# Performance work log

Hardware: AMD Instinct MI355X
Metric: run time of the kernel (lower is better)

## Reference

```python
import jax, jax.numpy as jnp
import numpy as np

K = 65536          # memory bank size
P = 4096           # partition_size
D = 256            # out_dim
E = 2              # num_experts_per_concept
SMOOTH = 0.1
NUM_TASKS = 1
B = 4096


def setup_inputs() -> dict:
    key = jax.random.key(0)
    k1, k2, k3 = jax.random.split(key, 3)
    queue = jax.random.normal(k1, (D, K), dtype=jnp.float32)
    queue = queue / jnp.linalg.norm(queue, axis=0, keepdims=True)  # normalize(dim=0)
    return {
        "student_embeds": jax.random.normal(k2, (B, D), dtype=jnp.float32),
        "teacher_embeds": jax.random.normal(k3, (B, D), dtype=jnp.float32),
        "queue": queue,
        "student_temp": 0.1,
        "teacher_temp": 0.04,
    }


def _one_task(queue, student_embeds, teacher_embeds, student_temp, teacher_temp, key):
    kperm, ksel = jax.random.split(key)
    # random partition of the bank (torch.randperm + split)
    perm = jax.random.permutation(kperm, K)
    part_idx, mem_idx = perm[:P], perm[P:]
    part = queue[:, part_idx]                      # [D, P]
    mem = queue[:, mem_idx]                        # [D, K-P]
    Kmp = K - P

    sims = part.T @ mem                            # [P, K-P]
    neigh_scores, neigh_idx = jax.lax.top_k(sims, E - 1)  # [P, E-1]

    # append self index (offset into concatenated [mem | part]) and 1-smoothing score
    idx_ = jnp.concatenate([neigh_idx, (Kmp + jnp.arange(P))[:, None]], axis=1)          # [P, E]
    scores_ = jnp.concatenate(
        [neigh_scores, jnp.full((P, 1), 1.0 - SMOOTH, dtype=sims.dtype)], axis=1)        # [P, E]

    # low_energy selection: multinomial(weights, P//2, replacement=False)
    P2 = P // 2
    m = jnp.mean(neigh_scores, axis=-1)            # [P]
    sample_means = jnp.abs(m)
    sample_stds = m                                 # (faithful to source: same quantity)
    coef = (sample_stds / (sample_means + 1e-8)) * (1.0 + 1.0 / (4.0 * Kmp))
    weights = 1.0 / coef                            # [P]
    # Gumbel top-k == multinomial without replacement proportional to weights
    gumbel = jax.random.gumbel(ksel, (P,))
    sel = jax.lax.top_k(jnp.log(weights) + gumbel, P2)[1]   # [P2]
    idx_ = idx_[sel]                                # [P2, E]
    scores_ = scores_[sel]                          # [P2, E]

    embeds_ = jnp.concatenate([mem, part], axis=1)  # [D, K]
    pne = embeds_[:, idx_.reshape(-1)]              # [D, P2*E] partition_neigh_embeddings

    sf = scores_.reshape(-1)                        # [P2*E]
    smooth_val = (1.0 - sf) / (P2 - 1)              # [P2*E]
    # partition_labels = arange(P).repeat_interleave(E)[:P2*E] == repeat(arange(P2), E)
    labels = jnp.repeat(jnp.arange(P2), E)          # [P2*E]
    M = jnp.broadcast_to(smooth_val[:, None], (P2 * E, P2))
    M = M.at[jnp.arange(P2 * E), labels].set(sf)    # scatter_ on dim 1
    M = M / M.sum(-1, keepdims=True)                # row-normalize

    s_probs = jax.nn.softmax(student_embeds @ pne / student_temp, axis=-1) @ M  # [B, P2]
    t_probs = jax.nn.softmax(teacher_embeds @ pne / teacher_temp, axis=-1) @ M  # [B, P2]
    return s_probs, t_probs


def reference(student_embeds, teacher_embeds, queue, student_temp, teacher_temp):
    base = jax.random.key(42)  # internal RNG (torch.randperm / multinomial equivalents)
    s_list, t_list = [], []
    for i in range(NUM_TASKS):
        s, t = _one_task(queue, student_embeds, teacher_embeds,
                         student_temp, teacher_temp, jax.random.fold_in(base, i))
        s_list.append(s)
        t_list.append(t)
    return jnp.stack(s_list), jnp.stack(t_list)  # each [NUM_TASKS, B, P//2]
```

## Files before the change

### kernel.cpp

```cpp
#include <hip/hip_runtime.h>
#include <cstdint>
#include <cmath>
#include <cstring>
#include <vector>
#include <algorithm>
#include <utility>

#define KTOT 65536
#define PP   4096
#define DD   256
#define KMP  61440
#define P2   2048
#define BB   4096
#define NPB  512
#define INVALID_C 0xFFFFFFFFu

static inline void tf2x32(uint32_t k0, uint32_t k1, uint32_t x0, uint32_t x1,
                          uint32_t* o0, uint32_t* o1) {
  static const uint32_t rot[2][4] = {{13u,15u,26u,6u},{17u,29u,16u,24u}};
  uint32_t ks[3] = {k0, k1, 0x1BD11BDAu ^ k0 ^ k1};
  uint32_t v0 = x0 + ks[0], v1 = x1 + ks[1];
  for (int i = 0; i < 5; ++i) {
    const uint32_t* r = rot[i & 1];
    for (int j = 0; j < 4; ++j) {
      v0 += v1;
      v1 = (v1 << r[j]) | (v1 >> (32u - r[j]));
      v1 ^= v0;
    }
    v0 += ks[(i + 1) % 3];
    v1 += ks[(i + 2) % 3] + (uint32_t)(i + 1);
  }
  *o0 = v0; *o1 = v1;
}

static inline uint32_t tf_bits32(uint32_t k0, uint32_t k1, uint32_t i) {
  uint32_t a, b;
  tf2x32(k0, k1, 0u, i, &a, &b);
  return a ^ b;
}

static uint32_t h_upload[KMP + KTOT + P2];
static uint32_t* const h_mem_idx    = h_upload;
static uint32_t* const h_pos_in_mem = h_upload + KMP;
static uint32_t* const h_partsel    = h_upload + KMP + KTOT;

static void host_prepare() {
  uint32_t f0, f1; tf2x32(0u, 42u, 0u, 0u, &f0, &f1);
  uint32_t kperm0, kperm1, ksel0, ksel1;
  tf2x32(f0, f1, 0u, 0u, &kperm0, &kperm1);
  tf2x32(f0, f1, 0u, 1u, &ksel0, &ksel1);

  std::vector<uint32_t> perm(KTOT);
  for (uint32_t i = 0; i < KTOT; ++i) perm[i] = i;
  std::vector<std::pair<uint32_t,uint32_t>> kv(KTOT);
  uint32_t key0 = kperm0, key1 = kperm1;
  for (int round = 0; round < 2; ++round) {
    uint32_t nk0, nk1, sk0, sk1;
    tf2x32(key0, key1, 0u, 0u, &nk0, &nk1);
    tf2x32(key0, key1, 0u, 1u, &sk0, &sk1);
    key0 = nk0; key1 = nk1;
    for (uint32_t i = 0; i < KTOT; ++i) {
      kv[i].first  = tf_bits32(sk0, sk1, i);
      kv[i].second = perm[i];
    }
    std::stable_sort(kv.begin(), kv.end(),
        [](const std::pair<uint32_t,uint32_t>& a,
           const std::pair<uint32_t,uint32_t>& b){ return a.first < b.first; });
    for (uint32_t i = 0; i < KTOT; ++i) perm[i] = kv[i].second;
  }
  static uint32_t part_idx[PP];
  for (int i = 0; i < PP;  ++i) part_idx[i] = perm[i];
  for (int i = 0; i < KMP; ++i) h_mem_idx[i] = perm[PP + i];
  for (int i = 0; i < KTOT; ++i) h_pos_in_mem[i] = INVALID_C;
  for (uint32_t c = 0; c < KMP; ++c) h_pos_in_mem[h_mem_idx[c]] = c;

  static float sval[PP];
  float c1f = (float)(1.0 + 1.0/(4.0*(double)KMP));
  float L0  = logf(1.0f / c1f);
  for (uint32_t i = 0; i < PP; ++i) {
    uint32_t bits = tf_bits32(ksel0, ksel1, i);
    uint32_t fb = (bits >> 9) | 0x3F800000u;
    float f; memcpy(&f, &fb, 4);
    f -= 1.0f;
    float u = (f == 0.0f) ? 1.17549435e-38f : f;
    float g = -logf(-logf(u));
    sval[i] = L0 + g;
  }
  static uint32_t order[PP];
  for (uint32_t i = 0; i < PP; ++i) order[i] = i;
  std::sort(order, order + PP, [](uint32_t a, uint32_t b){
    if (sval[a] != sval[b]) return sval[a] > sval[b];
    return a < b;
  });
  for (int k = 0; k < P2; ++k) h_partsel[k] = part_idx[order[k]];

  (void)hipHostRegister((void*)h_upload, sizeof(h_upload), hipHostRegisterDefault);
}

static const bool _host_tables_ready = (host_prepare(), true);

typedef __attribute__((ext_vector_type(8))) short bf16x8;
typedef __attribute__((ext_vector_type(4))) float f32x4;

__device__ inline unsigned short f2bf(float x) {
  union { float f; uint32_t u; } v; v.f = x;
  return (unsigned short)((v.u + 0x7FFFu + ((v.u >> 16) & 1u)) >> 16);
}

__device__ inline void gload16(const unsigned short* g, unsigned short* l) {
  __builtin_amdgcn_global_load_lds(
      (const __attribute__((address_space(1))) unsigned int*)g,
      (__attribute__((address_space(3))) unsigned int*)l, 16, 0, 0);
}

__device__ inline float wave_max(float v) {
#pragma unroll
  for (int off = 32; off > 0; off >>= 1) v = fmaxf(v, __shfl_xor(v, off, 64));
  return v;
}
__device__ inline float wave_sum(float v) {
#pragma unroll
  for (int off = 32; off > 0; off >>= 1) v += __shfl_xor(v, off, 64);
  return v;
}

__device__ __host__ inline int swz_g(int row) {
  return ((row >> 1) & 3) | (((row >> 3) & 1) << 3);
}
__device__ __host__ inline int swz(int row, int d) {
  return d ^ (swz_g(row) << 1);
}

__global__ __launch_bounds__(256)
void stageB_prep(const float* __restrict__ queue, const uint32_t* __restrict__ psel,
                 unsigned short* __restrict__ BhT, float* __restrict__ Apart,
                 unsigned short* __restrict__ AhT) {
  const int b = blockIdx.x;
  if (b < 4096) {
    __shared__ float t[64][65];
    const int tid = threadIdx.x;
    const int c4 = (tid & 15) * 4, r = tid >> 4;
    const int n0 = (b & 1023) * 64, d0 = (b >> 10) * 64;
#pragma unroll
    for (int i = 0; i < 4; ++i) {
      int d = r + i * 16;
      float4 v = *(const float4*)&queue[(d0 + d) * KTOT + n0 + c4];
      t[d][c4 + 0] = v.x; t[d][c4 + 1] = v.y; t[d][c4 + 2] = v.z; t[d][c4 + 3] = v.w;
    }
    __syncthreads();
#pragma unroll
    for (int i = 0; i < 4; ++i) {
      int n = r + i * 16;
      uint32_t lo = (uint32_t)f2bf(t[c4 + 0][n]) | ((uint32_t)f2bf(t[c4 + 1][n]) << 16);
      uint32_t hi = (uint32_t)f2bf(t[c4 + 2][n]) | ((uint32_t)f2bf(t[c4 + 3][n]) << 16);
      const int row = n0 + n;
      const int g = swz_g(row);
      const int pos = ((d0 + c4) ^ (g << 1)) & ~3;
      uint2 w;
      w.x = (g & 1) ? hi : lo;
      w.y = (g & 1) ? lo : hi;
      *(uint2*)&BhT[row * DD + pos] = w;
    }
  } else {
    int p = b - 4096, d = threadIdx.x;
    float q = queue[d * KTOT + (int)psel[p]];
    Apart[p * DD + d] = q;
    AhT[p * DD + swz(p, d)] = f2bf(q);
  }
}

__global__ __launch_bounds__(256)
void mfma_argmax(const unsigned short* __restrict__ AhT,
                 const unsigned short* __restrict__ BhT,
                 const uint32_t* __restrict__ pos_in_mem,
                 float* __restrict__ pv2, uint32_t* __restrict__ pc2) {
  __shared__ union SM {
    struct { unsigned short As[2][128][32]; unsigned short Bs[2][128][32]; } s;
    struct { float rv[128][33]; uint32_t ri[128][33]; } r;
  } sm;
  const int tid = threadIdx.x;

  const int flat = blockIdx.y * NPB + blockIdx.x;
  const int xcd = flat & 7, job = flat >> 3;
  const int nt = (xcd << 6) + (job >> 4);
  const int mt = job & 15;
  const int m0 = mt * 128, n0 = nt * 128;

  const int wave = tid >> 6, lane = tid & 63;
  const int wm = (wave >> 1) * 64, wn = (wave & 1) * 64;
  const int l15 = lane & 15, quad = lane >> 4;

  uint32_t carr[4];
#pragma unroll
  for (int j = 0; j < 4; ++j) carr[j] = pos_in_mem[n0 + wn + j * 16 + l15];

  const int gsw = swz_g(l15);
  const int o0 = (((quad << 2) | 0) ^ gsw) << 2;
  const int o1 = (((quad << 2) | 1) ^ gsw) << 2;
  const int o2 = (((quad << 2) | 2) ^ gsw) << 2;
  const int o3 = (((quad << 2) | 3) ^ gsw) << 2;

  f32x4 acc[4][4];
#pragma unroll
  for (int i = 0; i < 4; ++i)
#pragma unroll
    for (int j = 0; j < 4; ++j) acc[i][j] = (f32x4){0.f, 0.f, 0.f, 0.f};

  const int r4 = lane >> 2;
  const int c8 = (lane & 3) * 8;
  const unsigned short* gA0 = &AhT[(m0 + wave * 16 + r4) * DD + c8];
  const unsigned short* gA1 = gA0 + 64 * DD;
  const unsigned short* gB0 = &BhT[(n0 + wave * 16 + r4) * DD + c8];
  const unsigned short* gB1 = gB0 + 64 * DD;

  {
    unsigned short* lA = &sm.s.As[0][wave * 16][0];
    unsigned short* lB = &sm.s.Bs[0][wave * 16][0];
    gload16(gA0, lA); gload16(gA1, lA + 64 * 32);
    gload16(gB0, lB); gload16(gB1, lB + 64 * 32);
  }
  __syncthreads();

#pragma unroll
  for (int t = 0; t < 8; ++t) {
    const int cur = t & 1;
    if (t < 7) {
      const int k0 = (t + 1) * 32;
      unsigned short* lA = &sm.s.As[cur ^ 1][wave * 16][0];
      unsigned short* lB = &sm.s.Bs[cur ^ 1][wave * 16][0];
      gload16(gA0 + k0, lA); gload16(gA1 + k0, lA + 64 * 32);
      gload16(gB0 + k0, lB); gload16(gB1 + k0, lB + 64 * 32);
    }
    bf16x8 a[4], b[4];
#pragma unroll
    for (int i = 0; i < 4; ++i) {
      const char* rb = (const char*)&sm.s.As[cur][wm + i * 16 + l15][0];
      union { uint32_t u[4]; bf16x8 v; } f;
      f.u[0] = *(const uint32_t*)(rb + o0);
      f.u[1] = *(const uint32_t*)(rb + o1);
      f.u[2] = *(const uint32_t*)(rb + o2);
      f.u[3] = *(const uint32_t*)(rb + o3);
      a[i] = f.v;
    }
#pragma unroll
    for (int j = 0; j < 4; ++j) {
      const char* rb = (const char*)&sm.s.Bs[cur][wn + j * 16 + l15][0];
      union { uint32_t u[4]; bf16x8 v; } f;
      f.u[0] = *(const uint32_t*)(rb + o0);
      f.u[1] = *(const uint32_t*)(rb + o1);
      f.u[2] = *(const uint32_t*)(rb + o2);
      f.u[3] = *(const uint32_t*)(rb + o3);
      b[j] = f.v;
    }
#pragma unroll
    for (int i = 0; i < 4; ++i)
#pragma unroll
      for (int j = 0; j < 4; ++j)
        acc[i][j] = __builtin_amdgcn_mfma_f32_16x16x32_bf16(a[i], b[j], acc[i][j], 0, 0, 0);
    __syncthreads();
  }

#pragma unroll
  for (int i = 0; i < 4; ++i)
#pragma unroll
    for (int r = 0; r < 4; ++r) {
      float bv = -INFINITY; uint32_t bc = INVALID_C;
#pragma unroll
      for (int j = 0; j < 4; ++j) {
        float v = acc[i][j][r]; uint32_t c = carr[j];
        if (c != INVALID_C && (v > bv || (v == bv && c < bc))) { bv = v; bc = c; }
      }
      int row = wm + i * 16 + quad * 4 + r;
      sm.r.rv[row][(wave & 1) * 16 + l15] = bv;
      sm.r.ri[row][(wave & 1) * 16 + l15] = bc;
    }
  __syncthreads();
  if (tid < 128) {
    float v1 = -INFINITY, v2 = -INFINITY; uint32_t c1 = INVALID_C, c2 = INVALID_C;
#pragma unroll 4
    for (int s = 0; s < 32; ++s) {
      float v = sm.r.rv[tid][s]; uint32_t c = sm.r.ri[tid][s];
      if (c == INVALID_C) continue;
      if (v > v1 || (v == v1 && c < c1)) { v2 = v1; c2 = c1; v1 = v; c1 = c; }
      else if (v > v2 || (v == v2 && c < c2)) { v2 = v; c2 = c; }
    }
    int base = (m0 + tid) * (NPB * 2) + nt * 2;
    pv2[base] = v1;     pc2[base] = c1;
    pv2[base + 1] = v2; pc2[base + 1] = c2;
  }
}

#define EPS_W 0.01f
__global__ __launch_bounds__(256)
void argmax_rescore(const float* __restrict__ pv2, const uint32_t* __restrict__ pc2,
                    const float* __restrict__ Apart, const float* __restrict__ queue,
                    const uint32_t* __restrict__ mem_idx,
                    float* __restrict__ nval, uint32_t* __restrict__ nc) {
  __shared__ float wr[4];
  __shared__ uint32_t cand[32];
  __shared__ int cnt;
  __shared__ float bestv_s; __shared__ uint32_t bestc_s;
  const int row = blockIdx.x, tid = threadIdx.x;
  const int wave = tid >> 6;

  if (tid == 0) { cnt = 0; bestv_s = -INFINITY; bestc_s = INVALID_C; }
  float m = -INFINITY;
  for (int e = tid; e < NPB * 2; e += 256) m = fmaxf(m, pv2[row * (NPB * 2) + e]);
  m = wave_max(m);
  if ((tid & 63) == 0) wr[wave] = m;
  __syncthreads();
  const float M = fmaxf(fmaxf(wr[0], wr[1]), fmaxf(wr[2], wr[3]));
  for (int e = tid; e < NPB * 2; e += 256) {
    float v = pv2[row * (NPB * 2) + e]; uint32_t c = pc2[row * (NPB * 2) + e];
    if (c != INVALID_C && v >= M - EPS_W) {
      int k = atomicAdd(&cnt, 1);
      if (k < 32) cand[k] = c;
    }
  }
  __syncthreads();
  const int ncand = min(cnt, 32);
  const float av = Apart[row * DD + tid];
  for (int k = 0; k < ncand; ++k) {
    uint32_t c = cand[k];
    int n = (int)mem_idx[c];
    float p = wave_sum(av * queue[tid * KTOT + n]);
    if ((tid & 63) == 0) wr[wave] = p;
    __syncthreads();
    if (tid == 0) {
      float sc = wr[0] + wr[1] + wr[2] + wr[3];
      if (sc > bestv_s || (sc == bestv_s && c < bestc_s)) { bestv_s = sc; bestc_s = c; }
    }
    __syncthreads();
  }
  if (tid == 0) { nval[row] = bestv_s; nc[row] = bestc_s; }
}

__global__ __launch_bounds__(256)
void prep_ops(const float* __restrict__ S, const float* __restrict__ T,
              const float* __restrict__ queue,
              const uint32_t* __restrict__ nc, const float* __restrict__ nval,
              const uint32_t* __restrict__ mem_idx, const uint32_t* __restrict__ partsel,
              unsigned short* __restrict__ AhS, unsigned short* __restrict__ AlS,
              unsigned short* __restrict__ AhT2, unsigned short* __restrict__ AlT2,
              unsigned short* __restrict__ Bh, unsigned short* __restrict__ Bl,
              float* __restrict__ svp, float* __restrict__ dp) {
  const int b = blockIdx.x, d = threadIdx.x;
  if (b < 2 * BB) {
    const float* src = (b < BB) ? S : T;
    unsigned short* oh = (b < BB) ? AhS : AhT2;
    unsigned short* ol = (b < BB) ? AlS : AlT2;
    int row = b & (BB - 1);
    float v = src[row * DD + d];
    unsigned short hb = f2bf(v);
    float hf = __uint_as_float((uint32_t)hb << 16);
    unsigned short lb = f2bf(v - hf);
    int o = row * DD + swz(row, d);
    oh[o] = hb;
    ol[o] = lb;
  } else {
    int r = b - 2 * BB;
    int k = r >> 1;
    int idx = (r & 1) ? (int)partsel[k] : (int)mem_idx[nc[k]];
    float v = queue[d * KTOT + idx];
    unsigned short hb = f2bf(v);
    float hf = __uint_as_float((uint32_t)hb << 16);
    unsigned short lb = f2bf(v - hf);
    int o = r * DD + swz(r, d);
    Bh[o] = hb;
    Bl[o] = lb;
    if (!(r & 1) && d < 2) {
      float sf = (d == 0) ? nval[k] : 0.9f;
      float sv = (1.0f - sf) / 2047.0f;
      float rs = sf + 2047.0f * sv;
      svp[2 * k + d] = sv / rs;
      dp[2 * k + d]  = (sf - sv) / rs;
    }
  }
}

__global__ __launch_bounds__(256)
void gemm_split(const unsigned short* __restrict__ Ah,
                const unsigned short* __restrict__ Al,
                const unsigned short* __restrict__ Bh,
                const unsigned short* __restrict__ Bl,
                float* __restrict__ Fo) {
  __shared__ struct { unsigned short As[2][128][32]; unsigned short Bs[2][128][32]; } sm;
  const int tid = threadIdx.x;
  const int m0 = blockIdx.y * 128, n0 = blockIdx.x * 128;
  const int wave = tid >> 6, lane = tid & 63;
  const int wm = (wave >> 1) * 64, wn = (wave & 1) * 64;
  const int l15 = lane & 15, quad = lane >> 4;

  const int gsw = swz_g(l15);
  const int o0 = (((quad << 2) | 0) ^ gsw) << 2;
  const int o1 = (((quad << 2) | 1) ^ gsw) << 2;
  const int o2 = (((quad << 2) | 2) ^ gsw) << 2;
  const int o3 = (((quad << 2) | 3) ^ gsw) << 2;

  f32x4 acc[4][4];
#pragma unroll
  for (int i = 0; i < 4; ++i)
#pragma unroll
    for (int j = 0; j < 4; ++j) acc[i][j] = (f32x4){0.f, 0.f, 0.f, 0.f};

  const int r4 = lane >> 2;
  const int c8 = (lane & 3) * 8;
  const int aoff = (m0 + wave * 16 + r4) * DD + c8;
  const int boff = (n0 + wave * 16 + r4) * DD + c8;

  {
    unsigned short* lA = &sm.As[0][wave * 16][0];
    unsigned short* lB = &sm.Bs[0][wave * 16][0];
    gload16(Ah + aoff, lA); gload16(Ah + aoff + 64 * DD, lA + 64 * 32);
    gload16(Bh + boff, lB); gload16(Bh + boff + 64 * DD, lB + 64 * 32);
  }
  __syncthreads();

#pragma unroll 2
  for (int t = 0; t < 24; ++t) {
    const int cur = t & 1;
    if (t < 23) {
      const int tn = t + 1;
      const int p = tn >> 3, k0 = (tn & 7) * 32;
      const unsigned short* ga = ((p == 2) ? Al : Ah) + aoff + k0;
      const unsigned short* gb = ((p == 1) ? Bl : Bh) + boff + k0;
      unsigned short* lA = &sm.As[cur ^ 1][wave * 16][0];
      unsigned short* lB = &sm.Bs[cur ^ 1][wave * 16][0];
      gload16(ga, lA); gload16(ga + 64 * DD, lA + 64 * 32);
      gload16(gb, lB); gload16(gb + 64 * DD, lB + 64 * 32);
    }
    bf16x8 a[4], b[4];
#pragma unroll
    for (int i = 0; i < 4; ++i) {
      const char* rb = (const char*)&sm.As[cur][wm + i * 16 + l15][0];
      union { uint32_t u[4]; bf16x8 v; } f;
      f.u[0] = *(const uint32_t*)(rb + o0);
      f.u[1] = *(const uint32_t*)(rb + o1);
      f.u[2] = *(const uint32_t*)(rb + o2);
      f.u[3] = *(const uint32_t*)(rb + o3);
      a[i] = f.v;
    }
#pragma unroll
    for (int j = 0; j < 4; ++j) {
      const char* rb = (const char*)&sm.Bs[cur][wn + j * 16 + l15][0];
      union { uint32_t u[4]; bf16x8 v; } f;
      f.u[0] = *(const uint32_t*)(rb + o0);
      f.u[1] = *(const uint32_t*)(rb + o1);
      f.u[2] = *(const uint32_t*)(rb + o2);
      f.u[3] = *(const uint32_t*)(rb + o3);
      b[j] = f.v;
    }
#pragma unroll
    for (int i = 0; i < 4; ++i)
#pragma unroll
      for (int j = 0; j < 4; ++j)
        acc[i][j] = __builtin_amdgcn_mfma_f32_16x16x32_bf16(a[i], b[j], acc[i][j], 0, 0, 0);
    __syncthreads();
  }

#pragma unroll
  for (int i = 0; i < 4; ++i)
#pragma unroll
    for (int j = 0; j < 4; ++j)
#pragma unroll
      for (int r = 0; r < 4; ++r)
        Fo[(m0 + wm + i * 16 + quad * 4 + r) * PP + n0 + wn + j * 16 + l15] = acc[i][j][r];
}

__global__ __launch_bounds__(256)
void softmax_out(const float* __restrict__ F, const float* __restrict__ temp_ptr,
                 const float* __restrict__ svp, const float* __restrict__ dp,
                 float* __restrict__ out) {
  __shared__ float e[PP];
  __shared__ float wrm[4], wrz[4], wrs[4];
  int b = blockIdx.x, tid = threadIdx.x;
  const int wave = tid >> 6;
  const float invtemp = 1.0f / temp_ptr[0];
  float lv[PP / 256];
  float lmax = -INFINITY;
#pragma unroll
  for (int k = 0; k < PP / 256; ++k) {
    float l = F[b * PP + tid + k * 256] * invtemp;
    lv[k] = l;
    lmax = fmaxf(lmax, l);
  }
  lmax = wave_max(lmax);
  if ((tid & 63) == 0) wrm[wave] = lmax;
  __syncthreads();
  lmax = fmaxf(fmaxf(wrm[0], wrm[1]), fmaxf(wrm[2], wrm[3]));

  float z = 0.0f, sacc = 0.0f;
#pragma unroll
  for (int k = 0; k < PP / 256; ++k) {
    int r = tid + k * 256;
    float ev = __expf(lv[k] - lmax);
    e[r] = ev;
    z += ev;
    sacc = fmaf(ev, svp[r], sacc);
  }
  z = wave_sum(z);
  sacc = wave_sum(sacc);
  if ((tid & 63) == 0) { wrz[wave] = z; wrs[wave] = sacc; }
  __syncthreads();
  z = wrz[0] + wrz[1] + wrz[2] + wrz[3];
  sacc = wrs[0] + wrs[1] + wrs[2] + wrs[3];

  float invz = 1.0f / z;
  for (int j = tid; j < P2; j += 256) {
    float v = sacc + e[2 * j] * dp[2 * j] + e[2 * j + 1] * dp[2 * j + 1];
    out[b * P2 + j] = v * invz;
  }
}

#define OFF_BHT      0u
#define OFF_PV2      33554432u
#define OFF_PC2      41943040u
#define OFF_AHT      50331648u
#define OFF_APART    51380224u
#define OFF_F        0u
#define OFF_BH       33554432u
#define OFF_BL       35651584u
#define OFF_AHS      37748736u
#define OFF_ALS      39845888u
#define OFF_AHT2     41943040u
#define OFF_ALT2     44040192u
#define OFF_SVP      71303168u
#define OFF_DP       71319552u
#define OFF_NVAL     71352320u
#define OFF_NC       71360512u
#define OFF_UP_MEM   71368704u
#define OFF_UP_POS   71614464u
#define OFF_UP_PSEL  71876608u

extern "C" void kernel_launch(void* const* d_in, const int* in_sizes, int n_in,
                              void* d_out, int out_size, void* d_ws, size_t ws_size,
                              hipStream_t stream) {
  (void)in_sizes; (void)n_in; (void)out_size; (void)ws_size;
  (void)_host_tables_ready;
  const float* d_student = (const float*)d_in[0];
  const float* d_teacher = (const float*)d_in[1];
  const float* d_queue   = (const float*)d_in[2];
  const float* d_stemp   = (const float*)d_in[3];
  const float* d_ttemp   = (const float*)d_in[4];
  float* out = (float*)d_out;
  char* ws = (char*)d_ws;

  unsigned short* BhT   = (unsigned short*)(ws + OFF_BHT);
  float*          pv2   = (float*)(ws + OFF_PV2);
  uint32_t*       pc2   = (uint32_t*)(ws + OFF_PC2);
  unsigned short* AhT   = (unsigned short*)(ws + OFF_AHT);
  float*          Apart = (float*)(ws + OFF_APART);
  float*          F     = (float*)(ws + OFF_F);
  unsigned short* Bh    = (unsigned short*)(ws + OFF_BH);
  unsigned short* Bl    = (unsigned short*)(ws + OFF_BL);
  unsigned short* AhS   = (unsigned short*)(ws + OFF_AHS);
  unsigned short* AlS   = (unsigned short*)(ws + OFF_ALS);
  unsigned short* AhT2  = (unsigned short*)(ws + OFF_AHT2);
  unsigned short* AlT2  = (unsigned short*)(ws + OFF_ALT2);
  float*          svp   = (float*)(ws + OFF_SVP);
  float*          dp    = (float*)(ws + OFF_DP);
  float*          nval  = (float*)(ws + OFF_NVAL);
  uint32_t*       nc    = (uint32_t*)(ws + OFF_NC);
  uint32_t*       dMemIdx = (uint32_t*)(ws + OFF_UP_MEM);
  uint32_t*       dPosMem = (uint32_t*)(ws + OFF_UP_POS);
  uint32_t*       dPSel   = (uint32_t*)(ws + OFF_UP_PSEL);

  hipMemcpyAsync(dMemIdx, h_upload, sizeof(h_upload), hipMemcpyHostToDevice, stream);

  stageB_prep<<<4096 + P2, 256, 0, stream>>>(d_queue, dPSel, BhT, Apart, AhT);
  mfma_argmax<<<dim3(NPB, P2 / 128), 256, 0, stream>>>(AhT, BhT, dPosMem, pv2, pc2);
  argmax_rescore<<<P2, 256, 0, stream>>>(pv2, pc2, Apart, d_queue, dMemIdx, nval, nc);

  prep_ops<<<2 * BB + PP, 256, 0, stream>>>(d_student, d_teacher, d_queue,
      nc, nval, dMemIdx, dPSel, AhS, AlS, AhT2, AlT2, Bh, Bl, svp, dp);

  for (int half = 0; half < 2; ++half) {
    gemm_split<<<dim3(PP / 128, 2048 / 128), 256, 0, stream>>>(
        AhS + (size_t)half * 2048 * DD, AlS + (size_t)half * 2048 * DD, Bh, Bl, F);
    softmax_out<<<2048, 256, 0, stream>>>(F, d_stemp, svp, dp,
        out + (size_t)half * 2048 * P2);
  }
  for (int half = 0; half < 2; ++half) {
    gemm_split<<<dim3(PP / 128, 2048 / 128), 256, 0, stream>>>(
        AhT2 + (size_t)half * 2048 * DD, AlT2 + (size_t)half * 2048 * DD, Bh, Bl, F);
    softmax_out<<<2048, 256, 0, stream>>>(F, d_ttemp, svp, dp,
        out + (size_t)BB * P2 + (size_t)half * 2048 * P2);
  }
}
```

Before: 475.1 us.

## Quantize similarity-search GEMM to int8 MFMA with wider rescore tolerance

Converts the coarse nearest-neighbour similarity GEMM from bf16 to int8 quantized inputs (scale 127) using the i32 16x16x64 int8 MFMA, halving the bytes staged through LDS and the number of K iterations. Accumulators are rescaled to float before the per-row argmax, and the rescore tolerance window is widened to absorb the larger quantization error, with the exact fp32 rescore still deciding the final neighbour. The risk is that the coarser approximation pushes more candidates into the rescore window or misses the true argmax.

```diff
diff --git a/kernel.cpp b/kernel.cpp
--- a/kernel.cpp
+++ b/kernel.cpp
@@ -101,13 +101,14 @@
 
 typedef __attribute__((ext_vector_type(8))) short bf16x8;
 typedef __attribute__((ext_vector_type(4))) float f32x4;
+typedef __attribute__((ext_vector_type(4))) int   i32x4;
 
 __device__ inline unsigned short f2bf(float x) {
   union { float f; uint32_t u; } v; v.f = x;
   return (unsigned short)((v.u + 0x7FFFu + ((v.u >> 16) & 1u)) >> 16);
 }
 
-__device__ inline void gload16(const unsigned short* g, unsigned short* l) {
+__device__ inline void gload16(const void* g, void* l) {
   __builtin_amdgcn_global_load_lds(
       (const __attribute__((address_space(1))) unsigned int*)g,
       (__attribute__((address_space(3))) unsigned int*)l, 16, 0, 0);
@@ -130,11 +131,20 @@
 __device__ __host__ inline int swz(int row, int d) {
   return d ^ (swz_g(row) << 1);
 }
+__device__ __host__ inline int swz8(int row, int d) {
+  return d ^ (swz_g(row) << 2);
+}
+
+__device__ inline int q127(float v) {
+  return __float2int_rn(v * 127.0f);
+}
+
+#define SINV (1.0f / 16129.0f)
 
 __global__ __launch_bounds__(256)
 void stageB_prep(const float* __restrict__ queue, const uint32_t* __restrict__ psel,
-                 unsigned short* __restrict__ BhT, float* __restrict__ Apart,
-                 unsigned short* __restrict__ AhT) {
+                 signed char* __restrict__ Bi8, float* __restrict__ Apart,
+                 signed char* __restrict__ Ai8) {
   const int b = blockIdx.x;
   if (b < 4096) {
     __shared__ float t[64][65];
@@ -151,31 +161,28 @@
 #pragma unroll
     for (int i = 0; i < 4; ++i) {
       int n = r + i * 16;
-      uint32_t lo = (uint32_t)f2bf(t[c4 + 0][n]) | ((uint32_t)f2bf(t[c4 + 1][n]) << 16);
-      uint32_t hi = (uint32_t)f2bf(t[c4 + 2][n]) | ((uint32_t)f2bf(t[c4 + 3][n]) << 16);
       const int row = n0 + n;
-      const int g = swz_g(row);
-      const int pos = ((d0 + c4) ^ (g << 1)) & ~3;
-      uint2 w;
-      w.x = (g & 1) ? hi : lo;
-      w.y = (g & 1) ? lo : hi;
-      *(uint2*)&BhT[row * DD + pos] = w;
+      uint32_t w = 0;
+#pragma unroll
+      for (int q = 0; q < 4; ++q)
+        w |= ((uint32_t)(q127(t[c4 + q][n]) & 0xFF)) << (8 * q);
+      *(uint32_t*)&Bi8[row * DD + swz8(row, d0 + c4)] = w;
     }
   } else {
     int p = b - 4096, d = threadIdx.x;
     float q = queue[d * KTOT + (int)psel[p]];
     Apart[p * DD + d] = q;
-    AhT[p * DD + swz(p, d)] = f2bf(q);
+    Ai8[p * DD + swz8(p, d)] = (signed char)q127(q);
   }
 }
 
 __global__ __launch_bounds__(256)
-void mfma_argmax(const unsigned short* __restrict__ AhT,
-                 const unsigned short* __restrict__ BhT,
+void mfma_argmax(const signed char* __restrict__ Ai8,
+                 const signed char* __restrict__ Bi8,
                  const uint32_t* __restrict__ pos_in_mem,
                  float* __restrict__ pv2, uint32_t* __restrict__ pc2) {
   __shared__ union SM {
-    struct { unsigned short As[2][128][32]; unsigned short Bs[2][128][32]; } s;
+    struct { signed char As[2][128][64]; signed char Bs[2][128][64]; } s;
     struct { float rv[128][33]; uint32_t ri[128][33]; } r;
   } sm;
   const int tid = threadIdx.x;
@@ -200,63 +207,63 @@
   const int o2 = (((quad << 2) | 2) ^ gsw) << 2;
   const int o3 = (((quad << 2) | 3) ^ gsw) << 2;
 
-  f32x4 acc[4][4];
+  i32x4 acc[4][4];
 #pragma unroll
   for (int i = 0; i < 4; ++i)
 #pragma unroll
-    for (int j = 0; j < 4; ++j) acc[i][j] = (f32x4){0.f, 0.f, 0.f, 0.f};
+    for (int j = 0; j < 4; ++j) acc[i][j] = (i32x4){0, 0, 0, 0};
 
   const int r4 = lane >> 2;
-  const int c8 = (lane & 3) * 8;
-  const unsigned short* gA0 = &AhT[(m0 + wave * 16 + r4) * DD + c8];
-  const unsigned short* gA1 = gA0 + 64 * DD;
-  const unsigned short* gB0 = &BhT[(n0 + wave * 16 + r4) * DD + c8];
-  const unsigned short* gB1 = gB0 + 64 * DD;
+  const int c16 = (lane & 3) * 16;
+  const signed char* gA0 = &Ai8[(m0 + wave * 16 + r4) * DD + c16];
+  const signed char* gA1 = gA0 + 64 * DD;
+  const signed char* gB0 = &Bi8[(n0 + wave * 16 + r4) * DD + c16];
+  const signed char* gB1 = gB0 + 64 * DD;
 
   {
-    unsigned short* lA = &sm.s.As[0][wave * 16][0];
-    unsigned short* lB = &sm.s.Bs[0][wave * 16][0];
-    gload16(gA0, lA); gload16(gA1, lA + 64 * 32);
-    gload16(gB0, lB); gload16(gB1, lB + 64 * 32);
-  }
-  __syncthreads();
-
-#pragma unroll
-  for (int t = 0; t < 8; ++t) {
+    signed char* lA = &sm.s.As[0][wave * 16][0];
+    signed char* lB = &sm.s.Bs[0][wave * 16][0];
+    gload16(gA0, lA); gload16(gA1, lA + 64 * 64);
+    gload16(gB0, lB); gload16(gB1, lB + 64 * 64);
+  }
+  __syncthreads();
+
+#pragma unroll
+  for (int t = 0; t < 4; ++t) {
     const int cur = t & 1;
-    if (t < 7) {
-      const int k0 = (t + 1) * 32;
-      unsigned short* lA = &sm.s.As[cur ^ 1][wave * 16][0];
-      unsigned short* lB = &sm.s.Bs[cur ^ 1][wave * 16][0];
-      gload16(gA0 + k0, lA); gload16(gA1 + k0, lA + 64 * 32);
-      gload16(gB0 + k0, lB); gload16(gB1 + k0, lB + 64 * 32);
-    }
-    bf16x8 a[4], b[4];
+    if (t < 3) {
+      const int k0 = (t + 1) * 64;
+      signed char* lA = &sm.s.As[cur ^ 1][wave * 16][0];
+      signed char* lB = &sm.s.Bs[cur ^ 1][wave * 16][0];
+      gload16(gA0 + k0, lA); gload16(gA1 + k0, lA + 64 * 64);
+      gload16(gB0 + k0, lB); gload16(gB1 + k0, lB + 64 * 64);
+    }
+    i32x4 a[4], b[4];
 #pragma unroll
     for (int i = 0; i < 4; ++i) {
       const char* rb = (const char*)&sm.s.As[cur][wm + i * 16 + l15][0];
-      union { uint32_t u[4]; bf16x8 v; } f;
-      f.u[0] = *(const uint32_t*)(rb + o0);
-      f.u[1] = *(const uint32_t*)(rb + o1);
-      f.u[2] = *(const uint32_t*)(rb + o2);
-      f.u[3] = *(const uint32_t*)(rb + o3);
+      union { int u[4]; i32x4 v; } f;
+      f.u[0] = *(const int*)(rb + o0);
+      f.u[1] = *(const int*)(rb + o1);
+      f.u[2] = *(const int*)(rb + o2);
+      f.u[3] = *(const int*)(rb + o3);
       a[i] = f.v;
     }
 #pragma unroll
     for (int j = 0; j < 4; ++j) {
       const char* rb = (const char*)&sm.s.Bs[cur][wn + j * 16 + l15][0];
-      union { uint32_t u[4]; bf16x8 v; } f;
-      f.u[0] = *(const uint32_t*)(rb + o0);
-      f.u[1] = *(const uint32_t*)(rb + o1);
-      f.u[2] = *(const uint32_t*)(rb + o2);
-      f.u[3] = *(const uint32_t*)(rb + o3);
+      union { int u[4]; i32x4 v; } f;
+      f.u[0] = *(const int*)(rb + o0);
+      f.u[1] = *(const int*)(rb + o1);
+      f.u[2] = *(const int*)(rb + o2);
+      f.u[3] = *(const int*)(rb + o3);
       b[j] = f.v;
     }
 #pragma unroll
     for (int i = 0; i < 4; ++i)
 #pragma unroll
       for (int j = 0; j < 4; ++j)
-        acc[i][j] = __builtin_amdgcn_mfma_f32_16x16x32_bf16(a[i], b[j], acc[i][j], 0, 0, 0);
+        acc[i][j] = __builtin_amdgcn_mfma_i32_16x16x64_i8(a[i], b[j], acc[i][j], 0, 0, 0);
     __syncthreads();
   }
 
@@ -267,7 +274,7 @@
       float bv = -INFINITY; uint32_t bc = INVALID_C;
 #pragma unroll
       for (int j = 0; j < 4; ++j) {
-        float v = acc[i][j][r]; uint32_t c = carr[j];
+        float v = (float)acc[i][j][r] * SINV; uint32_t c = carr[j];
         if (c != INVALID_C && (v > bv || (v == bv && c < bc))) { bv = v; bc = c; }
       }
       int row = wm + i * 16 + quad * 4 + r;
@@ -290,7 +297,7 @@
   }
 }
 
-#define EPS_W 0.01f
+#define EPS_W 0.025f
 __global__ __launch_bounds__(256)
 void argmax_rescore(const float* __restrict__ pv2, const uint32_t* __restrict__ pc2,
                     const float* __restrict__ Apart, const float* __restrict__ queue,
@@ -545,10 +552,10 @@
   float* out = (float*)d_out;
   char* ws = (char*)d_ws;
 
-  unsigned short* BhT   = (unsigned short*)(ws + OFF_BHT);
+  signed char*    Bi8   = (signed char*)(ws + OFF_BHT);
   float*          pv2   = (float*)(ws + OFF_PV2);
   uint32_t*       pc2   = (uint32_t*)(ws + OFF_PC2);
-  unsigned short* AhT   = (unsigned short*)(ws + OFF_AHT);
+  signed char*    Ai8   = (signed char*)(ws + OFF_AHT);
   float*          Apart = (float*)(ws + OFF_APART);
   float*          F     = (float*)(ws + OFF_F);
   unsigned short* Bh    = (unsigned short*)(ws + OFF_BH);
@@ -567,8 +574,8 @@
 
   hipMemcpyAsync(dMemIdx, h_upload, sizeof(h_upload), hipMemcpyHostToDevice, stream);
 
-  stageB_prep<<<4096 + P2, 256, 0, stream>>>(d_queue, dPSel, BhT, Apart, AhT);
-  mfma_argmax<<<dim3(NPB, P2 / 128), 256, 0, stream>>>(AhT, BhT, dPosMem, pv2, pc2);
+  stageB_prep<<<4096 + P2, 256, 0, stream>>>(d_queue, dPSel, Bi8, Apart, Ai8);
+  mfma_argmax<<<dim3(NPB, P2 / 128), 256, 0, stream>>>(Ai8, Bi8, dPosMem, pv2, pc2);
   argmax_rescore<<<P2, 256, 0, stream>>>(pv2, pc2, Apart, d_queue, dMemIdx, nval, nc);
 
   prep_ops<<<2 * BB + PP, 256, 0, stream>>>(d_student, d_teacher, d_queue,
```

Measured after the change: 473.5 us. Within noise of the previous version (-0.3%).
